# Kernel tuning notes

Measured on AMD Instinct MI355X. Metric: run time of the kernel, lower is better.

The kernel has to match this reference:

```python
import jax, jax.numpy as jnp
import numpy as np

B, N, S = 8, 4096, 1024
D1, D2 = 128, 256
IN_C = D1 + D2
MLP = [256, 256]
BN_EPS = 1e-5


def setup_inputs() -> dict:
    key = jax.random.key(0)
    ks = jax.random.split(key, 32)
    inp = {
        'xyz1': jax.random.uniform(ks[0], (B, 3, N), dtype=jnp.float32),
        'xyz2': jax.random.uniform(ks[1], (B, 3, S), dtype=jnp.float32),
        'points1': jax.random.normal(ks[2], (B, D1, N), dtype=jnp.float32),
        'points2': jax.random.normal(ks[3], (B, D2, S), dtype=jnp.float32),
        'colors1': jax.random.normal(ks[4], (B, D1, N), dtype=jnp.float32),
        'colors2': jax.random.normal(ks[5], (B, D2, S), dtype=jnp.float32),
    }
    # conv1x1 + BN params for the two MLP stacks (points / colors)
    k = 6
    last = IN_C
    for li, out_c in enumerate(MLP, start=1):
        for tag in ('p', 'c'):
            scale = 1.0 / np.sqrt(last)
            inp[f'W{tag}{li}'] = jax.random.uniform(ks[k], (out_c, last), jnp.float32, -scale, scale); k += 1
            inp[f'b{tag}{li}'] = jax.random.uniform(ks[k], (out_c,), jnp.float32, -scale, scale); k += 1
            inp[f'g{tag}{li}'] = jnp.ones((out_c,), jnp.float32)
            inp[f'be{tag}{li}'] = jnp.zeros((out_c,), jnp.float32)
        last = out_c
    return inp


def _square_distance(src, dst):
    # src [B,N,3], dst [B,S,3] -> [B,N,S]
    d = -2.0 * jnp.einsum('bnc,bsc->bns', src, dst)
    d = d + jnp.sum(src * src, -1)[:, :, None]
    d = d + jnp.sum(dst * dst, -1)[:, None, :]
    return d


def _three_interp(xyz1, xyz2, feat2):
    # xyz1 [B,N,3], xyz2 [B,S,3], feat2 [B,S,D] -> [B,N,D]
    dists = _square_distance(xyz1, xyz2)              # [B,N,S]
    neg_d3, idx = jax.lax.top_k(-dists, 3)            # smallest 3 distances
    d3 = -neg_d3                                      # [B,N,3] ascending
    recip = 1.0 / (d3 + 1e-8)
    weight = recip / jnp.sum(recip, axis=2, keepdims=True)
    gathered = jax.vmap(lambda f, i: f[i])(feat2, idx)  # [B,N,3,D]
    return jnp.sum(gathered * weight[..., None], axis=2)


def _conv_bn_relu(x, W, b, g, be):
    # x [B,N,Cin]; conv1x1 == per-point linear; BN in training mode (batch stats)
    y = jnp.einsum('bnc,oc->bno', x, W) + b
    m = jnp.mean(y, axis=(0, 1))
    v = jnp.var(y, axis=(0, 1))
    yn = (y - m) * jax.lax.rsqrt(v + BN_EPS)
    return jax.nn.relu(yn * g + be)


def reference(xyz1, xyz2, points1, points2, colors1, colors2,
              Wp1, bp1, gp1, bep1, Wc1, bc1, gc1, bec1,
              Wp2, bp2, gp2, bep2, Wc2, bc2, gc2, bec2):
    x1 = jnp.transpose(xyz1, (0, 2, 1))   # [B,N,3]
    x2 = jnp.transpose(xyz2, (0, 2, 1))   # [B,S,3]
    p2 = jnp.transpose(points2, (0, 2, 1))  # [B,S,D2]
    c2 = jnp.transpose(colors2, (0, 2, 1))

    interp_p = _three_interp(x1, x2, p2)  # [B,N,D2]
    interp_c = _three_interp(x1, x2, c2)

    p1 = jnp.transpose(points1, (0, 2, 1))  # [B,N,D1]
    c1 = jnp.transpose(colors1, (0, 2, 1))
    new_p = jnp.concatenate([p1, interp_p], axis=-1)  # [B,N,IN_C]
    new_c = jnp.concatenate([c1, interp_c], axis=-1)

    new_p = _conv_bn_relu(new_p, Wp1, bp1, gp1, bep1)
    new_p = _conv_bn_relu(new_p, Wp2, bp2, gp2, bep2)
    new_c = _conv_bn_relu(new_c, Wc1, bc1, gc1, bec1)
    new_c = _conv_bn_relu(new_c, Wc2, bc2, gc2, bec2)

    return (jnp.transpose(new_p, (0, 2, 1)), jnp.transpose(new_c, (0, 2, 1)))
```

## Files before the change

### kernel.cpp

```cpp
#include <hip/hip_runtime.h>
#include <cstdint>
#include <cstddef>


#define B_   8
#define N_   4096
#define S_   1024
#define D1_  128
#define D2_  256
#define INC_ 384
#define OC_  256
#define M_   (B_ * N_)

typedef __attribute__((ext_vector_type(8))) short sh8;
typedef __attribute__((ext_vector_type(4))) float f32x4;
typedef __attribute__((ext_vector_type(4))) unsigned short ush4;
typedef __attribute__((ext_vector_type(8))) unsigned short ush8;

__device__ __forceinline__ unsigned short bf16rne(float f) {
    union { float f; unsigned u; } v; v.f = f;
    return (unsigned short)((v.u + 0x7FFFu + ((v.u >> 16) & 1u)) >> 16);
}
__device__ __forceinline__ float bf2f(unsigned short h) {
    union { unsigned u; float f; } v; v.u = ((unsigned)h) << 16;
    return v.f;
}
__device__ __forceinline__ void gload16(const void* gsrc, void* lds) {
    __builtin_amdgcn_global_load_lds(
        (const __attribute__((address_space(1))) void*)gsrc,
        (__attribute__((address_space(3))) void*)lds, 16, 0, 0);
}

#define INS(pd, pi) { \
    bool l0 = (pd < d0) || (pd == d0 && pi < i0); \
    bool l1 = (pd < d1) || (pd == d1 && pi < i1); \
    bool l2 = (pd < d2) || (pd == d2 && pi < i2); \
    d2 = l1 ? d1 : (l2 ? pd : d2);  i2 = l1 ? i1 : (l2 ? pi : i2); \
    d1 = l0 ? d0 : (l1 ? pd : d1);  i1 = l0 ? i0 : (l1 ? pi : i1); \
    d0 = l0 ? pd : d0;              i0 = l0 ? pi : i0; \
}

__global__ __launch_bounds__(256) void front_kernel(
    const float* __restrict__ xyz1, const float* __restrict__ xyz2,
    const float* __restrict__ points1, const float* __restrict__ colors1,
    const float* __restrict__ points2, const float* __restrict__ colors2,
    const float* __restrict__ Wp1, const float* __restrict__ Wc1,
    const float* __restrict__ Wp2, const float* __restrict__ Wc2,
    int* __restrict__ idxo, float* __restrict__ wo,
    unsigned short* __restrict__ p2b, unsigned short* __restrict__ c2b,
    unsigned short* __restrict__ Wb1, unsigned short* __restrict__ Wb2,
    unsigned short* __restrict__ Xp)
{
    __shared__ __align__(16) char fsm[17664];
    const int bid = blockIdx.x;
    const int tid = threadIdx.x;

    if (bid < 1024) {
        float4* sc = (float4*)fsm;
        const int b = bid >> 7, qb = bid & 127;
        const float* x2 = xyz2 + (size_t)b * 3 * S_;
        for (int s = tid; s < S_; s += 256) {
            float xs = x2[s], ys = x2[S_ + s], zs = x2[2 * S_ + s];
            sc[s] = make_float4(xs, ys, zs, xs * xs + ys * ys + zs * zs);
        }
        __syncthreads();
        const int q = qb * 32 + (tid >> 3);
        const int sub = tid & 7;
        const float* x1 = xyz1 + (size_t)b * 3 * N_;
        const float xq = x1[q], yq = x1[N_ + q], zq = x1[2 * N_ + q];
        const float n1 = xq * xq + yq * yq + zq * zq;
        float d0 = 3.4e38f, d1 = 3.4e38f, d2 = 3.4e38f;
        int i0 = 0, i1 = 0, i2 = 0;
#pragma unroll 4
        for (int j = 0; j < 128; ++j) {
            int s = j * 8 + sub;
            float4 v = sc[s];
            float dot = xq * v.x + yq * v.y + zq * v.z;
            float d = (n1 - 2.0f * dot) + v.w;
            bool c0 = d < d0, c1 = d < d1, c2 = d < d2;
            d2 = c1 ? d1 : (c2 ? d : d2); i2 = c1 ? i1 : (c2 ? s : i2);
            d1 = c0 ? d0 : (c1 ? d : d1); i1 = c0 ? i0 : (c1 ? s : i1);
            d0 = c0 ? d : d0;             i0 = c0 ? s : i0;
        }
#pragma unroll
        for (int off = 1; off < 8; off <<= 1) {
            float pd0 = __shfl_xor(d0, off), pd1 = __shfl_xor(d1, off), pd2 = __shfl_xor(d2, off);
            int   pi0 = __shfl_xor(i0, off), pi1 = __shfl_xor(i1, off), pi2 = __shfl_xor(i2, off);
            INS(pd0, pi0) INS(pd1, pi1) INS(pd2, pi2)
        }
        if (sub == 0) {
            float r0 = 1.f / (d0 + 1e-8f);
            float r1 = 1.f / (d1 + 1e-8f);
            float r2 = 1.f / (d2 + 1e-8f);
            float rs = r0 + r1 + r2;
            int base = (b * N_ + q) * 3;
            idxo[base] = i0; idxo[base + 1] = i1; idxo[base + 2] = i2;
            wo[base] = r0 / rs; wo[base + 1] = r1 / rs; wo[base + 2] = r2 / rs;
        }
    } else if (bid < 5120) {
        float (*tile)[33] = (float(*)[33])fsm;
        const int u = bid - 1024;
        const int which = u >> 11;
        const int v = u & 2047;
        const int z = v >> 8, rem = v & 255;
        const int cx = rem & 31, ry = rem >> 5;
        const int tx = tid & 31, ty = tid >> 5;
        const float* s = (which ? colors2 : points2) + (size_t)z * D2_ * S_;
        unsigned short* d = (which ? c2b : p2b) + (size_t)z * S_ * D2_;
#pragma unroll
        for (int i = 0; i < 4; ++i)
            tile[ty + i * 8][tx] = s[(size_t)(ry * 32 + ty + i * 8) * S_ + cx * 32 + tx];
        __syncthreads();
#pragma unroll
        for (int i = 0; i < 4; ++i)
            d[(size_t)(cx * 32 + ty + i * 8) * D2_ + ry * 32 + tx] =
                bf16rne(tile[tx][ty + i * 8]);
    } else if (bid < 5440) {
        int e = ((bid - 5120) * 256 + tid) * 4;
        const float* src; unsigned short* dst; int off;
        if (e < 98304)       { src = Wp1; dst = Wb1;          off = e; }
        else if (e < 196608) { src = Wc1; dst = Wb1 + 98304;  off = e - 98304; }
        else if (e < 262144) { src = Wp2; dst = Wb2;          off = e - 196608; }
        else                 { src = Wc2; dst = Wb2 + 65536;  off = e - 262144; }
        float4 v = *(const float4*)(src + off);
        ush4 o; o[0] = bf16rne(v.x); o[1] = bf16rne(v.y); o[2] = bf16rne(v.z); o[3] = bf16rne(v.w);
        *(ush4*)(dst + off) = o;
    } else {
        float (*tileA)[69] = (float(*)[69])fsm;
        const int u = bid - 5440;
        const int t = u >> 9, rem = u & 511;
        const int b = rem >> 6, n0 = (rem & 63) * 64;
        const float* x1 = t ? colors1 : points1;
        size_t mbase = (size_t)t * M_ + (size_t)b * N_ + n0;
#pragma unroll
        for (int ph = 0; ph < 2; ++ph) {
            if (ph) __syncthreads();
#pragma unroll
            for (int it = 0; it < 4; ++it) {
                int fl4 = it * 256 + tid;
                int dl = fl4 >> 4, nl = (fl4 & 15) * 4;
                float4 v = *(const float4*)(x1 + ((size_t)b * D1_ + ph * 64 + dl) * N_ + n0 + nl);
                tileA[nl][dl] = v.x; tileA[nl + 1][dl] = v.y;
                tileA[nl + 2][dl] = v.z; tileA[nl + 3][dl] = v.w;
            }
            __syncthreads();
#pragma unroll
            for (int it = 0; it < 2; ++it) {
                int e8 = it * 256 + tid;
                int r = e8 >> 3, dc = (e8 & 7) * 8;
                ush8 o;
#pragma unroll
                for (int j = 0; j < 8; ++j) o[j] = bf16rne(tileA[r][dc + j]);
                *(ush8*)(Xp + (mbase + r) * D1_ + ph * 64 + dc) = o;
            }
        }
    }
}

__global__ __launch_bounds__(512, 2) void gemm1f_kernel(
    const unsigned short* __restrict__ Xp,
    const unsigned short* __restrict__ p2b,
    const unsigned short* __restrict__ c2b,
    const int* __restrict__ idxw, const float* __restrict__ wgtw,
    const unsigned short* __restrict__ Wb1,
    unsigned short* __restrict__ Y1,
    float* __restrict__ psum, float* __restrict__ psq)
{
    const int wg  = blockIdx.x;
    const int xcd = wg & 7;
    const int t   = xcd & 1;
    const int mt  = (xcd >> 1) * 32 + (wg >> 3);
    const int m0  = mt * 256;
    const int bb  = m0 >> 12;
    const unsigned short* Aw  = Wb1 + (size_t)t * (OC_ * INC_);
    const unsigned short* Xb  = Xp + (size_t)t * M_ * D1_;
    const unsigned short* f2b = t ? c2b : p2b;

    __shared__ __align__(16) char smem[131072];

    const int tid  = threadIdx.x;
    const int lane = tid & 63;
    const int wid  = tid >> 6;
    const int wc   = wid & 3;
    const int wm   = wid >> 2;
    const int srow = tid >> 3;
    const int k8   = (tid & 7) * 8;
    const int sk   = ((tid & 7) ^ (srow & 7)) * 8;
    const int kgrp = (lane >> 4) * 16;

    int gi[4][3]; float gw[4][3];
#pragma unroll
    for (int p = 0; p < 4; ++p) {
        int base = (m0 + p * 64 + srow) * 3;
#pragma unroll
        for (int j = 0; j < 3; ++j) { gi[p][j] = idxw[base + j]; gw[p][j] = wgtw[base + j]; }
    }

    f32x4 acc[4][8];
#pragma unroll
    for (int i = 0; i < 4; ++i)
#pragma unroll
        for (int j = 0; j < 8; ++j) acc[i][j] = f32x4{0.f, 0.f, 0.f, 0.f};

    auto stageA = [&](int buf, int kc) {
#pragma unroll
        for (int p = 0; p < 4; ++p)
            gload16(Aw + (size_t)(p * 64 + srow) * INC_ + kc + sk,
                    smem + buf * 32768 + p * 8192 + wid * 1024);
    };
    auto stageBX = [&](int buf, int kc) {
#pragma unroll
        for (int p = 0; p < 4; ++p)
            gload16(Xb + (size_t)(m0 + p * 64 + srow) * D1_ + kc + sk,
                    smem + 65536 + buf * 32768 + p * 8192 + wid * 1024);
    };
    auto stageBG = [&](int buf, int kc) {
        const int d0k = kc - D1_ + k8;
#pragma unroll
        for (int p = 0; p < 4; ++p) {
            int row = p * 64 + srow;
            ush8 a0 = *(const ush8*)(f2b + ((size_t)bb * S_ + gi[p][0]) * D2_ + d0k);
            ush8 a1 = *(const ush8*)(f2b + ((size_t)bb * S_ + gi[p][1]) * D2_ + d0k);
            ush8 a2 = *(const ush8*)(f2b + ((size_t)bb * S_ + gi[p][2]) * D2_ + d0k);
            ush8 ov;
#pragma unroll
            for (int j = 0; j < 8; ++j)
                ov[j] = bf16rne(gw[p][0] * bf2f(a0[j]) + gw[p][1] * bf2f(a1[j])
                              + gw[p][2] * bf2f(a2[j]));
            *(ush8*)(smem + 65536 + buf * 32768 + row * 128
                     + ((k8 * 2) ^ ((row & 7) << 4))) = ov;
        }
    };
    auto compute = [&](int buf) {
#pragma unroll
        for (int kk = 0; kk < 2; ++kk) {
            sh8 a[4], b[8];
#pragma unroll
            for (int f = 0; f < 4; ++f) {
                int ra = wc * 64 + (lane & 15) + f * 16;
                a[f] = *(const sh8*)(smem + buf * 32768 + ra * 128
                        + ((kk * 64 + kgrp) ^ ((ra & 7) << 4)));
            }
#pragma unroll
            for (int f = 0; f < 8; ++f) {
                int rb = wm * 128 + (lane & 15) + f * 16;
                b[f] = *(const sh8*)(smem + 65536 + buf * 32768 + rb * 128
                        + ((kk * 64 + kgrp) ^ ((rb & 7) << 4)));
            }
#pragma unroll
            for (int fc = 0; fc < 4; ++fc)
#pragma unroll
                for (int fm = 0; fm < 8; ++fm)
                    acc[fc][fm] = __builtin_amdgcn_mfma_f32_16x16x32_bf16(
                        a[fc], b[fm], acc[fc][fm], 0, 0, 0);
        }
    };

    stageA(0, 0); stageBX(0, 0);
    __syncthreads();
    int cur = 0;
    for (int step = 0; step < 6; ++step) {
        int kcn = (step + 1) * 64;
        if (step < 5) {
            stageA(cur ^ 1, kcn);
            if (kcn < D1_) stageBX(cur ^ 1, kcn);
            else           stageBG(cur ^ 1, kcn);
        }
        compute(cur);
        __syncthreads();
        cur ^= 1;
    }

    const int mrow = m0 + wm * 128 + (lane & 15);
    const int chq  = (lane >> 4) * 4;
#pragma unroll
    for (int fm = 0; fm < 8; ++fm)
#pragma unroll
        for (int fc = 0; fc < 4; ++fc) {
            ush4 v;
#pragma unroll
            for (int r = 0; r < 4; ++r) v[r] = bf16rne(acc[fc][fm][r]);
            *(ush4*)(Y1 + ((size_t)t * M_ + mrow + fm * 16) * OC_
                      + wc * 64 + fc * 16 + chq) = v;
        }

    float* sArr = (float*)smem;
    const int contrib = wm * 16 + (lane & 15);
#pragma unroll
    for (int ph = 0; ph < 2; ++ph) {
#pragma unroll
        for (int fc = 0; fc < 4; ++fc) {
            f32x4 s4;
#pragma unroll
            for (int r = 0; r < 4; ++r) {
                float s = 0.f;
#pragma unroll
                for (int fm = 0; fm < 8; ++fm) { float v = acc[fc][fm][r]; s += ph ? v * v : v; }
                s4[r] = s;
            }
            *(f32x4*)&sArr[contrib * 264 + wc * 64 + fc * 16 + chq] = s4;
        }
        __syncthreads();
        if (tid < 256) {
            float s = 0.f;
#pragma unroll
            for (int k = 0; k < 32; ++k) s += sArr[((k + tid) & 31) * 264 + tid];
            (ph ? psq : psum)[((size_t)t * 128 + mt) * 256 + tid] = s;
        }
        __syncthreads();
    }
}

__global__ __launch_bounds__(256) void reduce_kernel(
    const float* __restrict__ psum, const float* __restrict__ psq,
    const float* __restrict__ gp, const float* __restrict__ bep,
    const float* __restrict__ gc, const float* __restrict__ bec,
    float* __restrict__ ss, int layerOff)
{
    const int t = blockIdx.x, cs = blockIdx.y;
    const int tid = threadIdx.x;
    const int cl = tid & 63, grp = tid >> 6;
    const int c = cs * 64 + cl;
    float s = 0.f, q = 0.f;
    for (int k = grp; k < 128; k += 4) {
        s += psum[((size_t)t * 128 + k) * 256 + c];
        q += psq [((size_t)t * 128 + k) * 256 + c];
    }
    __shared__ float ls[4][64], lq[4][64];
    ls[grp][cl] = s; lq[grp][cl] = q;
    __syncthreads();
    if (tid < 64) {
        s = ls[0][cl] + ls[1][cl] + ls[2][cl] + ls[3][cl];
        q = lq[0][cl] + lq[1][cl] + lq[2][cl] + lq[3][cl];
        float mean = s * (1.f / (float)M_);
        float var  = q * (1.f / (float)M_) - mean * mean;
        float inv  = rsqrtf(var + 1e-5f);
        float g = (t ? gc : gp)[c], be = (t ? bec : bep)[c];
        float sc = g * inv;
        ss[layerOff + t * 256 + c]       = sc;
        ss[layerOff + 512 + t * 256 + c] = be - mean * sc;
    }
}

__global__ __launch_bounds__(512, 2) void gemm2f_kernel(
    const unsigned short* __restrict__ Y1,
    const unsigned short* __restrict__ Wb2,
    const float* __restrict__ ss,
    unsigned short* __restrict__ y2b,
    float* __restrict__ psum, float* __restrict__ psq)
{
    const int t  = blockIdx.y;
    const int m0 = blockIdx.x * 256;
    const unsigned short* Aw = Wb2 + (size_t)t * (OC_ * OC_);
    const unsigned short* By = Y1 + (size_t)t * M_ * OC_;

    __shared__ __align__(16) char smem[131072];
    __shared__ float Slds[256], Hlds[256];

    const int tid  = threadIdx.x;
    const int lane = tid & 63;
    const int wid  = tid >> 6;
    const int wc   = wid & 3;
    const int wm   = wid >> 2;
    const int srow = tid >> 3;
    const int k8   = (tid & 7) * 8;
    const int sk   = ((tid & 7) ^ (srow & 7)) * 8;
    const int kgrp = (lane >> 4) * 16;

    if (tid < 256) { Slds[tid] = ss[t * 256 + tid]; Hlds[tid] = ss[512 + t * 256 + tid]; }
    __syncthreads();

    f32x4 acc[4][8];
#pragma unroll
    for (int i = 0; i < 4; ++i)
#pragma unroll
        for (int j = 0; j < 8; ++j) acc[i][j] = f32x4{0.f, 0.f, 0.f, 0.f};

    auto stageA = [&](int buf, int kc) {
#pragma unroll
        for (int p = 0; p < 4; ++p)
            gload16(Aw + (size_t)(p * 64 + srow) * OC_ + kc + sk,
                    smem + buf * 32768 + p * 8192 + wid * 1024);
    };
    auto stageBY = [&](int buf, int kc) {
#pragma unroll
        for (int p = 0; p < 4; ++p) {
            int row = p * 64 + srow;
            ush8 yv = *(const ush8*)(By + (size_t)(m0 + row) * OC_ + kc + k8);
            ush8 ov;
#pragma unroll
            for (int j = 0; j < 8; ++j) {
                float y = bf2f(yv[j]);
                ov[j] = bf16rne(fmaxf(0.f, fmaf(y, Slds[kc + k8 + j], Hlds[kc + k8 + j])));
            }
            *(ush8*)(smem + 65536 + buf * 32768 + row * 128
                     + ((k8 * 2) ^ ((row & 7) << 4))) = ov;
        }
    };
    auto compute = [&](int buf) {
#pragma unroll
        for (int kk = 0; kk < 2; ++kk) {
            sh8 a[4], b[8];
#pragma unroll
            for (int f = 0; f < 4; ++f) {
                int ra = wc * 64 + (lane & 15) + f * 16;
                a[f] = *(const sh8*)(smem + buf * 32768 + ra * 128
                        + ((kk * 64 + kgrp) ^ ((ra & 7) << 4)));
            }
#pragma unroll
            for (int f = 0; f < 8; ++f) {
                int rb = wm * 128 + (lane & 15) + f * 16;
                b[f] = *(const sh8*)(smem + 65536 + buf * 32768 + rb * 128
                        + ((kk * 64 + kgrp) ^ ((rb & 7) << 4)));
            }
#pragma unroll
            for (int fc = 0; fc < 4; ++fc)
#pragma unroll
                for (int fm = 0; fm < 8; ++fm)
                    acc[fc][fm] = __builtin_amdgcn_mfma_f32_16x16x32_bf16(
                        a[fc], b[fm], acc[fc][fm], 0, 0, 0);
        }
    };

    stageA(0, 0); stageBY(0, 0);
    __syncthreads();
    int cur = 0;
    for (int step = 0; step < 4; ++step) {
        int kcn = (step + 1) * 64;
        if (step < 3) { stageA(cur ^ 1, kcn); stageBY(cur ^ 1, kcn); }
        compute(cur);
        __syncthreads();
        cur ^= 1;
    }

    const int mrow = m0 + wm * 128 + (lane & 15);
    const int chq  = (lane >> 4) * 4;
#pragma unroll
    for (int fm = 0; fm < 8; ++fm)
#pragma unroll
        for (int fc = 0; fc < 4; ++fc) {
            ush4 v;
#pragma unroll
            for (int r = 0; r < 4; ++r) v[r] = bf16rne(acc[fc][fm][r]);
            *(ush4*)(y2b + ((size_t)t * M_ + mrow + fm * 16) * OC_
                      + wc * 64 + fc * 16 + chq) = v;
        }

    float* sArr = (float*)smem;
    const int contrib = wm * 16 + (lane & 15);
#pragma unroll
    for (int ph = 0; ph < 2; ++ph) {
#pragma unroll
        for (int fc = 0; fc < 4; ++fc) {
            f32x4 s4;
#pragma unroll
            for (int r = 0; r < 4; ++r) {
                float s = 0.f;
#pragma unroll
                for (int fm = 0; fm < 8; ++fm) { float v = acc[fc][fm][r]; s += ph ? v * v : v; }
                s4[r] = s;
            }
            *(f32x4*)&sArr[contrib * 264 + wc * 64 + fc * 16 + chq] = s4;
        }
        __syncthreads();
        if (tid < 256) {
            float s = 0.f;
#pragma unroll
            for (int k = 0; k < 32; ++k) s += sArr[((k + tid) & 31) * 264 + tid];
            (ph ? psq : psum)[((size_t)t * 128 + blockIdx.x) * 256 + tid] = s;
        }
        __syncthreads();
    }
}

__global__ __launch_bounds__(256) void bnT_kernel(
    const unsigned short* __restrict__ y2b, const float* __restrict__ ss,
    float* __restrict__ out)
{
    const int z = blockIdx.z;
    const int t = z >> 3, b = z & 7;
    const int o0 = blockIdx.y * 64;
    const int n0 = blockIdx.x * 64;
    const int tid = threadIdx.x;
    __shared__ unsigned short tile[64][72];

    const unsigned short* src = y2b + ((size_t)t * M_ + (size_t)b * N_ + n0) * OC_ + o0;
#pragma unroll
    for (int it = 0; it < 2; ++it) {
        int u = it * 256 + tid;
        int m_l = u >> 3, o8 = (u & 7) * 8;
        *(ush8*)&tile[m_l][o8] = *(const ush8*)(src + (size_t)m_l * OC_ + o8);
    }
    __syncthreads();
#pragma unroll
    for (int it = 0; it < 4; ++it) {
        int v = it * 256 + tid;
        int o_l = v >> 4, n4 = (v & 15) * 4;
        int o = o0 + o_l;
        float sc = ss[1024 + t * 256 + o];
        float sh = ss[1536 + t * 256 + o];
        float4 w;
        w.x = fmaxf(0.f, fmaf(bf2f(tile[n4][o_l]),     sc, sh));
        w.y = fmaxf(0.f, fmaf(bf2f(tile[n4 + 1][o_l]), sc, sh));
        w.z = fmaxf(0.f, fmaf(bf2f(tile[n4 + 2][o_l]), sc, sh));
        w.w = fmaxf(0.f, fmaf(bf2f(tile[n4 + 3][o_l]), sc, sh));
        *(float4*)(out + (((size_t)t * B_ + b) * OC_ + o) * N_ + n0 + n4) = w;
    }
}

extern "C" void kernel_launch(void* const* d_in, const int* in_sizes, int n_in,
                              void* d_out, int out_size, void* d_ws, size_t ws_size,
                              hipStream_t stream)
{
    const float* xyz1    = (const float*)d_in[0];
    const float* xyz2    = (const float*)d_in[1];
    const float* points1 = (const float*)d_in[2];
    const float* points2 = (const float*)d_in[3];
    const float* colors1 = (const float*)d_in[4];
    const float* colors2 = (const float*)d_in[5];
    const float* Wp1  = (const float*)d_in[6];
    const float* gp1  = (const float*)d_in[8];
    const float* bep1 = (const float*)d_in[9];
    const float* Wc1  = (const float*)d_in[10];
    const float* gc1  = (const float*)d_in[12];
    const float* bec1 = (const float*)d_in[13];
    const float* Wp2  = (const float*)d_in[14];
    const float* gp2  = (const float*)d_in[16];
    const float* bep2 = (const float*)d_in[17];
    const float* Wc2  = (const float*)d_in[18];
    const float* gc2  = (const float*)d_in[20];
    const float* bec2 = (const float*)d_in[21];

    char* ws = (char*)d_ws;
    unsigned short* y2b  = (unsigned short*)(ws + 0);
    unsigned short* Xp   = (unsigned short*)(ws + 0);
    unsigned short* p2b  = (unsigned short*)(ws + 16777216);
    unsigned short* c2b  = (unsigned short*)(ws + 20971520);
    int*   idxw = (int*)  (ws + 25165824);
    float* wgtw = (float*)(ws + 25559040);
    unsigned short* Y1   = (unsigned short*)(ws + 33554432);
    unsigned short* Wb1  = (unsigned short*)(ws + 67108864);
    unsigned short* Wb2  = (unsigned short*)(ws + 67895296);
    float* psum = (float*)(ws + 68419584);
    float* psq  = (float*)(ws + 68681728);
    float* ssb  = (float*)(ws + 68943872);
    float* out  = (float*)d_out;

    front_kernel<<<6464, 256, 0, stream>>>(xyz1, xyz2, points1, colors1,
                                           points2, colors2, Wp1, Wc1, Wp2, Wc2,
                                           idxw, wgtw, p2b, c2b, Wb1, Wb2, Xp);
    gemm1f_kernel<<<256, 512, 0, stream>>>(Xp, p2b, c2b, idxw, wgtw,
                                           Wb1, Y1, psum, psq);
    reduce_kernel<<<dim3(2, 4), 256, 0, stream>>>(psum, psq, gp1, bep1, gc1, bec1, ssb, 0);
    gemm2f_kernel<<<dim3(128, 2), 512, 0, stream>>>(Y1, Wb2, ssb, y2b, psum, psq);
    reduce_kernel<<<dim3(2, 4), 256, 0, stream>>>(psum, psq, gp2, bep2, gc2, bec2, ssb, 1024);
    bnT_kernel<<<dim3(64, 4, 16), 256, 0, stream>>>(y2b, ssb, out);
}
```

Measured before the change: 113.9 us.

## Fuse BN statistic reduction into GEMM kernels via last-block atomic counter

Removes the two separate reduce_kernel launches. Each GEMM block now writes its partial sums with agent-scope stores and bumps an atomic counter, and the last block per branch reduces all partials and writes the BN scale and shift. The counter is zeroed in front_kernel and reset after use. This saves two kernel launches and their gaps, at the cost of a serialized tail reduction in one block and extra fence and atomic overhead.

After: 141.6 us. 1.24x slower.

```diff
diff --git a/kernel.cpp b/kernel.cpp
--- a/kernel.cpp
+++ b/kernel.cpp
@@ -29,6 +29,12 @@
     __builtin_amdgcn_global_load_lds(
         (const __attribute__((address_space(1))) void*)gsrc,
         (__attribute__((address_space(3))) void*)lds, 16, 0, 0);
+}
+__device__ __forceinline__ void st_agent(float* p, float v) {
+    __hip_atomic_store(p, v, __ATOMIC_RELAXED, __HIP_MEMORY_SCOPE_AGENT);
+}
+__device__ __forceinline__ float ld_agent(const float* p) {
+    return __hip_atomic_load(p, __ATOMIC_RELAXED, __HIP_MEMORY_SCOPE_AGENT);
 }
 
 #define INS(pd, pi) { \
@@ -49,7 +55,7 @@
     int* __restrict__ idxo, float* __restrict__ wo,
     unsigned short* __restrict__ p2b, unsigned short* __restrict__ c2b,
     unsigned short* __restrict__ Wb1, unsigned short* __restrict__ Wb2,
-    unsigned short* __restrict__ Xp)
+    unsigned short* __restrict__ Xp, unsigned int* __restrict__ cnt)
 {
     __shared__ __align__(16) char fsm[17664];
     const int bid = blockIdx.x;
@@ -116,6 +122,8 @@
             d[(size_t)(cx * 32 + ty + i * 8) * D2_ + ry * 32 + tx] =
                 bf16rne(tile[tx][ty + i * 8]);
     } else if (bid < 5440) {
+        if (bid == 5120 && tid < 4)
+            __hip_atomic_store(cnt + tid, 0u, __ATOMIC_RELAXED, __HIP_MEMORY_SCOPE_AGENT);
         int e = ((bid - 5120) * 256 + tid) * 4;
         const float* src; unsigned short* dst; int off;
         if (e < 98304)       { src = Wp1; dst = Wb1;          off = e; }
@@ -164,7 +172,10 @@
     const int* __restrict__ idxw, const float* __restrict__ wgtw,
     const unsigned short* __restrict__ Wb1,
     unsigned short* __restrict__ Y1,
-    float* __restrict__ psum, float* __restrict__ psq)
+    float* __restrict__ psum, float* __restrict__ psq,
+    const float* __restrict__ gp, const float* __restrict__ bep,
+    const float* __restrict__ gc, const float* __restrict__ bec,
+    float* __restrict__ ssb, unsigned int* __restrict__ cnt)
 {
     const int wg  = blockIdx.x;
     const int xcd = wg & 7;
@@ -177,6 +188,7 @@
     const unsigned short* f2b = t ? c2b : p2b;
 
     __shared__ __align__(16) char smem[131072];
+    __shared__ int isLast;
 
     const int tid  = threadIdx.x;
     const int lane = tid & 63;
@@ -305,49 +317,54 @@
             float s = 0.f;
 #pragma unroll
             for (int k = 0; k < 32; ++k) s += sArr[((k + tid) & 31) * 264 + tid];
-            (ph ? psq : psum)[((size_t)t * 128 + mt) * 256 + tid] = s;
-        }
-        __syncthreads();
-    }
-}
-
-__global__ __launch_bounds__(256) void reduce_kernel(
-    const float* __restrict__ psum, const float* __restrict__ psq,
-    const float* __restrict__ gp, const float* __restrict__ bep,
-    const float* __restrict__ gc, const float* __restrict__ bec,
-    float* __restrict__ ss, int layerOff)
-{
-    const int t = blockIdx.x, cs = blockIdx.y;
-    const int tid = threadIdx.x;
-    const int cl = tid & 63, grp = tid >> 6;
-    const int c = cs * 64 + cl;
-    float s = 0.f, q = 0.f;
-    for (int k = grp; k < 128; k += 4) {
-        s += psum[((size_t)t * 128 + k) * 256 + c];
-        q += psq [((size_t)t * 128 + k) * 256 + c];
-    }
-    __shared__ float ls[4][64], lq[4][64];
-    ls[grp][cl] = s; lq[grp][cl] = q;
+            st_agent(&(ph ? psq : psum)[((size_t)t * 128 + mt) * 256 + tid], s);
+        }
+        __syncthreads();
+    }
+
+    if (tid == 0) {
+        __threadfence();
+        unsigned old = __hip_atomic_fetch_add(cnt + t, 1u, __ATOMIC_ACQ_REL,
+                                              __HIP_MEMORY_SCOPE_AGENT);
+        isLast = (old == 127u);
+    }
     __syncthreads();
-    if (tid < 64) {
-        s = ls[0][cl] + ls[1][cl] + ls[2][cl] + ls[3][cl];
-        q = lq[0][cl] + lq[1][cl] + lq[2][cl] + lq[3][cl];
-        float mean = s * (1.f / (float)M_);
-        float var  = q * (1.f / (float)M_) - mean * mean;
-        float inv  = rsqrtf(var + 1e-5f);
-        float g = (t ? gc : gp)[c], be = (t ? bec : bep)[c];
-        float sc = g * inv;
-        ss[layerOff + t * 256 + c]       = sc;
-        ss[layerOff + 512 + t * 256 + c] = be - mean * sc;
+    if (isLast) {
+        const int ch = tid & 255, half = tid >> 8;
+        float s = 0.f, q = 0.f;
+        for (int k = half * 64; k < half * 64 + 64; ++k) {
+            s += ld_agent(&psum[((size_t)t * 128 + k) * 256 + ch]);
+            q += ld_agent(&psq [((size_t)t * 128 + k) * 256 + ch]);
+        }
+        float* sL = (float*)smem;
+        float* qL = (float*)(smem + 2048);
+        sL[half * 256 + ch] = s; qL[half * 256 + ch] = q;
+        __syncthreads();
+        if (tid < 256) {
+            s = sL[tid] + sL[256 + tid];
+            q = qL[tid] + qL[256 + tid];
+            float mean = s * (1.f / (float)M_);
+            float var  = q * (1.f / (float)M_) - mean * mean;
+            float inv  = rsqrtf(var + 1e-5f);
+            float g = (t ? gc : gp)[tid], be = (t ? bec : bep)[tid];
+            float sc = g * inv;
+            ssb[t * 256 + tid]       = sc;
+            ssb[512 + t * 256 + tid] = be - mean * sc;
+        }
+        if (tid == 0)
+            __hip_atomic_store(cnt + t, 0u, __ATOMIC_RELAXED, __HIP_MEMORY_SCOPE_AGENT);
     }
 }
 
 __global__ __launch_bounds__(512, 2) void gemm2f_kernel(
     const unsigned short* __restrict__ Y1,
     const unsigned short* __restrict__ Wb2,
-    const float* __restrict__ ss,
+    float* __restrict__ ss,
     unsigned short* __restrict__ y2b,
-    float* __restrict__ psum, float* __restrict__ psq)
+    float* __restrict__ psum, float* __restrict__ psq,
+    const float* __restrict__ gp, const float* __restrict__ bep,
+    const float* __restrict__ gc, const float* __restrict__ bec,
+    unsigned int* __restrict__ cnt)
 {
     const int t  = blockIdx.y;
     const int m0 = blockIdx.x * 256;
@@ -356,6 +373,7 @@
 
     __shared__ __align__(16) char smem[131072];
     __shared__ float Slds[256], Hlds[256];
+    __shared__ int isLast;
 
     const int tid  = threadIdx.x;
     const int lane = tid & 63;
@@ -467,9 +485,42 @@
             float s = 0.f;
 #pragma unroll
             for (int k = 0; k < 32; ++k) s += sArr[((k + tid) & 31) * 264 + tid];
-            (ph ? psq : psum)[((size_t)t * 128 + blockIdx.x) * 256 + tid] = s;
-        }
-        __syncthreads();
+            st_agent(&(ph ? psq : psum)[((size_t)t * 128 + blockIdx.x) * 256 + tid], s);
+        }
+        __syncthreads();
+    }
+
+    if (tid == 0) {
+        __threadfence();
+        unsigned old = __hip_atomic_fetch_add(cnt + 2 + t, 1u, __ATOMIC_ACQ_REL,
+                                              __HIP_MEMORY_SCOPE_AGENT);
+        isLast = (old == 127u);
+    }
+    __syncthreads();
+    if (isLast) {
+        const int ch = tid & 255, half = tid >> 8;
+        float s = 0.f, q = 0.f;
+        for (int k = half * 64; k < half * 64 + 64; ++k) {
+            s += ld_agent(&psum[((size_t)t * 128 + k) * 256 + ch]);
+            q += ld_agent(&psq [((size_t)t * 128 + k) * 256 + ch]);
+        }
+        float* sL = (float*)smem;
+        float* qL = (float*)(smem + 2048);
+        sL[half * 256 + ch] = s; qL[half * 256 + ch] = q;
+        __syncthreads();
+        if (tid < 256) {
+            s = sL[tid] + sL[256 + tid];
+            q = qL[tid] + qL[256 + tid];
+            float mean = s * (1.f / (float)M_);
+            float var  = q * (1.f / (float)M_) - mean * mean;
+            float inv  = rsqrtf(var + 1e-5f);
+            float g = (t ? gc : gp)[tid], be = (t ? bec : bep)[tid];
+            float sc = g * inv;
+            ss[1024 + t * 256 + tid] = sc;
+            ss[1536 + t * 256 + tid] = be - mean * sc;
+        }
+        if (tid == 0)
+            __hip_atomic_store(cnt + 2 + t, 0u, __ATOMIC_RELAXED, __HIP_MEMORY_SCOPE_AGENT);
     }
 }
 
@@ -544,15 +595,16 @@
     float* psum = (float*)(ws + 68419584);
     float* psq  = (float*)(ws + 68681728);
     float* ssb  = (float*)(ws + 68943872);
+    unsigned int* cnt = (unsigned int*)(ws + 68952064);
     float* out  = (float*)d_out;
 
     front_kernel<<<6464, 256, 0, stream>>>(xyz1, xyz2, points1, colors1,
                                            points2, colors2, Wp1, Wc1, Wp2, Wc2,
-                                           idxw, wgtw, p2b, c2b, Wb1, Wb2, Xp);
+                                           idxw, wgtw, p2b, c2b, Wb1, Wb2, Xp, cnt);
     gemm1f_kernel<<<256, 512, 0, stream>>>(Xp, p2b, c2b, idxw, wgtw,
-                                           Wb1, Y1, psum, psq);
-    reduce_kernel<<<dim3(2, 4), 256, 0, stream>>>(psum, psq, gp1, bep1, gc1, bec1, ssb, 0);
-    gemm2f_kernel<<<dim3(128, 2), 512, 0, stream>>>(Y1, Wb2, ssb, y2b, psum, psq);
-    reduce_kernel<<<dim3(2, 4), 256, 0, stream>>>(psum, psq, gp2, bep2, gc2, bec2, ssb, 1024);
+                                           Wb1, Y1, psum, psq,
+                                           gp1, bep1, gc1, bec1, ssb, cnt);
+    gemm2f_kernel<<<dim3(128, 2), 512, 0, stream>>>(Y1, Wb2, ssb, y2b, psum, psq,
+                                                    gp2, bep2, gc2, bec2, cnt);
     bnT_kernel<<<dim3(64, 4, 16), 256, 0, stream>>>(y2b, ssb, out);
 }
```
